# Performance work log

Hardware: AMD Instinct MI355X
Metric: run time of the kernel (lower is better)

The kernel has to match this reference:

```python
import jax, jax.numpy as jnp
import numpy as np

B, T, D_IN = 8, 1024, 320
L, H, DK, DV, DM, DI = 6, 8, 64, 64, 512, 2048


def _pe_table():
    pos = np.arange(T, dtype=np.float32)[:, None]
    div = np.exp(np.arange(0, DM, 2, dtype=np.float32) * (-np.log(10000.0) / DM))
    pe = np.zeros((T, DM), np.float32)
    pe[:, 0::2] = np.sin(pos * div)
    pe[:, 1::2] = np.cos(pos * div)
    return jnp.asarray(pe)


def setup_inputs() -> dict:
    key = jax.random.key(0)
    ks = jax.random.split(key, 16)
    rn = lambda k, shape, std: (jax.random.normal(k, shape, jnp.float32) * std)
    inp = {}
    inp["padded_input"] = jax.random.normal(ks[0], (B, T, D_IN), jnp.float32)
    inp["input_lengths"] = jax.random.randint(ks[1], (B,), T // 2, T + 1)
    # input projection + input layernorm (weights stored as [in, out])
    inp["w_in"] = rn(ks[2], (D_IN, DM), 0.02)
    inp["b_in"] = jnp.zeros((DM,), jnp.float32)
    inp["ln_in_g"] = jnp.ones((DM,), jnp.float32)
    inp["ln_in_b"] = jnp.zeros((DM,), jnp.float32)
    inp["pe"] = _pe_table()
    # stacked per-layer params, leading dim L
    inp["wq"] = rn(ks[3], (L, DM, H * DK), np.sqrt(2.0 / (DM + DK)))
    inp["bq"] = jnp.zeros((L, H * DK), jnp.float32)
    inp["wk"] = rn(ks[4], (L, DM, H * DK), np.sqrt(2.0 / (DM + DK)))
    inp["bk"] = jnp.zeros((L, H * DK), jnp.float32)
    inp["wv"] = rn(ks[5], (L, DM, H * DV), np.sqrt(2.0 / (DM + DV)))
    inp["bv"] = jnp.zeros((L, H * DV), jnp.float32)
    inp["wfc"] = rn(ks[6], (L, H * DV, DM), np.sqrt(2.0 / (H * DV + DM)))
    inp["bfc"] = jnp.zeros((L, DM), jnp.float32)
    inp["ln1_g"] = jnp.ones((L, DM), jnp.float32)
    inp["ln1_b"] = jnp.zeros((L, DM), jnp.float32)
    inp["w1"] = rn(ks[7], (L, DM, DI), np.sqrt(2.0 / (DM + DI)))
    inp["b1"] = jnp.zeros((L, DI), jnp.float32)
    inp["w2"] = rn(ks[8], (L, DI, DM), np.sqrt(2.0 / (DM + DI)))
    inp["b2"] = jnp.zeros((L, DM), jnp.float32)
    inp["ln2_g"] = jnp.ones((L, DM), jnp.float32)
    inp["ln2_b"] = jnp.zeros((L, DM), jnp.float32)
    return inp


def _layer_norm(x, g, b):
    mu = jnp.mean(x, axis=-1, keepdims=True)
    var = jnp.var(x, axis=-1, keepdims=True)
    return (x - mu) * jax.lax.rsqrt(var + 1e-5) * g + b


def _encoder(padded_input, input_lengths, w_in, b_in, ln_in_g, ln_in_b, pe,
             wq, bq, wk, bk, wv, bv, wfc, bfc, ln1_g, ln1_b,
             w1, b1, w2, b2, ln2_g, ln2_b):
    pos = jnp.arange(T)
    key_pad = pos[None, :] >= input_lengths[:, None]          # [B,T] True at pad
    non_pad = (~key_pad).astype(padded_input.dtype)[:, :, None]  # [B,T,1]
    scale = 1.0 / jnp.sqrt(jnp.float32(DK))

    x = _layer_norm(padded_input @ w_in + b_in, ln_in_g, ln_in_b) + pe[None]

    def body(x, p):
        Wq, Bq, Wk, Bk, Wv, Bv, Wfc, Bfc, G1, Bn1, W1, Bf1, W2, Bf2, G2, Bn2 = p
        res = x
        q = (x @ Wq + Bq).reshape(B, T, H, DK)
        k = (x @ Wk + Bk).reshape(B, T, H, DK)
        v = (x @ Wv + Bv).reshape(B, T, H, DV)
        attn = jnp.einsum('bqhd,bkhd->bhqk', q, k) * scale
        attn = jnp.where(key_pad[:, None, None, :], -jnp.inf, attn)
        attn = jax.nn.softmax(attn, axis=-1)
        o = jnp.einsum('bhqk,bkhd->bqhd', attn, v).reshape(B, T, H * DV)
        x = _layer_norm(o @ Wfc + Bfc + res, G1, Bn1) * non_pad
        res = x
        h = jax.nn.relu(x @ W1 + Bf1)
        x = _layer_norm(h @ W2 + Bf2 + res, G2, Bn2) * non_pad
        return x, None

    x, _ = jax.lax.scan(body, x, (wq, bq, wk, bk, wv, bv, wfc, bfc,
                                  ln1_g, ln1_b, w1, b1, w2, b2, ln2_g, ln2_b))
    return x


def reference(padded_input, input_lengths, w_in, b_in, ln_in_g, ln_in_b, pe,
              wq, bq, wk, bk, wv, bv, wfc, bfc, ln1_g, ln1_b,
              w1, b1, w2, b2, ln2_g, ln2_b):
    # dropout is identity in eval mode
    return _encoder(padded_input, input_lengths, w_in, b_in, ln_in_g, ln_in_b, pe,
                    wq, bq, wk, bk, wv, bv, wfc, bfc, ln1_g, ln1_b,
                    w1, b1, w2, b2, ln2_g, ln2_b)
```

## Files before the change

kernel.cpp:

```cpp
#include <hip/hip_runtime.h>
#include <hip/hip_bf16.h>


typedef unsigned short bh16;
typedef __bf16 bf16x8 __attribute__((ext_vector_type(8)));
typedef float f32x4 __attribute__((ext_vector_type(4)));
typedef unsigned int u32x4 __attribute__((ext_vector_type(4)));
typedef unsigned int u32x2 __attribute__((ext_vector_type(2)));

#define DEVI static __device__ __forceinline__

DEVI bh16 f2bf(float f) {
  union { float f; unsigned u; } x; x.f = f;
  unsigned r = x.u + 0x7fffu + ((x.u >> 16) & 1u);
  return (bh16)(r >> 16);
}
DEVI float bf2f(bh16 u) {
  union { unsigned u; float f; } x; x.u = ((unsigned)u) << 16; return x.f;
}
DEVI bf16x8 ld16(const bh16* p) {
  return __builtin_bit_cast(bf16x8, *(const u32x4*)p);
}
DEVI bf16x8 ld16b(const char* p) {
  return __builtin_bit_cast(bf16x8, *(const u32x4*)p);
}
DEVI f32x4 mfma16(bf16x8 a, bf16x8 b, f32x4 c) {
  return __builtin_amdgcn_mfma_f32_16x16x32_bf16(a, b, c, 0, 0, 0);
}
DEVI void async16(const void* g, void* l) {
  __builtin_amdgcn_global_load_lds(
      (const __attribute__((address_space(1))) void*)g,
      (__attribute__((address_space(3))) void*)l, 16, 0, 0);
}

DEVI void tcvt_body(const float* in, bh16* out, int K, int N, int n0, int k0) {
  __shared__ float t[32][33];
  int tx = threadIdx.x & 31, ty = threadIdx.x >> 5;
#pragma unroll
  for (int i = 0; i < 4; i++)
    t[ty + 8 * i][tx] = in[(size_t)(k0 + ty + 8 * i) * N + n0 + tx];
  __syncthreads();
#pragma unroll
  for (int i = 0; i < 4; i++)
    out[(size_t)(n0 + ty + 8 * i) * K + k0 + tx] = f2bf(t[tx][ty + 8 * i]);
}

__global__ __launch_bounds__(256) void tcvt_all(
    const float* __restrict__ w_in, const float* __restrict__ wq,
    const float* __restrict__ wk, const float* __restrict__ wv,
    const float* __restrict__ wfc, const float* __restrict__ w1,
    const float* __restrict__ w2, bh16* __restrict__ WinT,
    bh16* __restrict__ WqkvT, bh16* __restrict__ WfcT,
    bh16* __restrict__ W1T, bh16* __restrict__ W2T) {
  int p = blockIdx.x;
  const float* in; bh16* out; int K, N, rem;
  if (p < 160) {
    in = w_in; out = WinT; K = 320; N = 512; rem = p;
  } else if (p < 160 + 1536) {
    rem = p - 160; int l = rem >> 8; rem &= 255;
    in = wq + (size_t)l * 512 * 512; out = WqkvT + (size_t)l * 1536 * 512;
    K = 512; N = 512;
  } else if (p < 160 + 3072) {
    rem = p - 160 - 1536; int l = rem >> 8; rem &= 255;
    in = wk + (size_t)l * 512 * 512;
    out = WqkvT + (size_t)l * 1536 * 512 + (size_t)512 * 512;
    K = 512; N = 512;
  } else if (p < 160 + 4608) {
    rem = p - 160 - 3072; int l = rem >> 8; rem &= 255;
    in = wv + (size_t)l * 512 * 512;
    out = WqkvT + (size_t)l * 1536 * 512 + (size_t)1024 * 512;
    K = 512; N = 512;
  } else if (p < 160 + 6144) {
    rem = p - 160 - 4608; int l = rem >> 8; rem &= 255;
    in = wfc + (size_t)l * 512 * 512; out = WfcT + (size_t)l * 512 * 512;
    K = 512; N = 512;
  } else if (p < 160 + 6144 + 6144) {
    rem = p - 160 - 6144; int l = rem >> 10; rem &= 1023;
    in = w1 + (size_t)l * 512 * 2048; out = W1T + (size_t)l * 2048 * 512;
    K = 512; N = 2048;
  } else {
    rem = p - 160 - 12288; int l = rem >> 10; rem &= 1023;
    in = w2 + (size_t)l * 2048 * 512; out = W2T + (size_t)l * 512 * 2048;
    K = 2048; N = 512;
  }
  int nt = N >> 5;
  int n0 = (rem % nt) * 32, k0 = (rem / nt) * 32;
  tcvt_body(in, out, K, N, n0, k0);
}

__global__ __launch_bounds__(256) void bcat(
    const float* __restrict__ bq, const float* __restrict__ bk,
    const float* __restrict__ bv, float* __restrict__ out) {
  int l = blockIdx.x;
  for (int j = threadIdx.x; j < 1536; j += 256) {
    float v = (j < 512) ? bq[l * 512 + j]
            : (j < 1024) ? bk[l * 512 + j - 512] : bv[l * 512 + j - 1024];
    out[l * 1536 + j] = v;
  }
}

__global__ __launch_bounds__(256) void cvt_in(
    const float* __restrict__ in, bh16* __restrict__ out, int n4) {
  int i = blockIdx.x * 256 + threadIdx.x;
  if (i < n4) {
    float4 v = ((const float4*)in)[i];
    u32x2 pk;
    pk[0] = (unsigned)f2bf(v.x) | ((unsigned)f2bf(v.y) << 16);
    pk[1] = (unsigned)f2bf(v.z) | ((unsigned)f2bf(v.w) << 16);
    *(u32x2*)(out + (size_t)i * 4) = pk;
  }
}

template <int BM, int BN, int RELU, int OUTF32, int QKV>
__global__ __launch_bounds__(256) void gemm_bt(
    const bh16* __restrict__ A, const bh16* __restrict__ Bt,
    const float* __restrict__ bias, void* __restrict__ Cout,
    bh16* __restrict__ vtOut, const int* __restrict__ lens,
    int M, int N, int K) {
  constexpr int BK = 64;
  constexpr int PX = (8192 / BM) / 8;
  constexpr int PXS = (PX == 8) ? 3 : 4;
  __shared__ __align__(16) bh16 As[2][BM * BK];
  __shared__ __align__(16) bh16 Bs[2][BN * BK];
  const int tid = threadIdx.x;
  const int wave = tid >> 6, lane = tid & 63;
  const int lq = lane & 15, grp = lane >> 4;
  const int p = blockIdx.x;
  const int xcd = p & 7, idx = p >> 3;
  const int m0 = (((idx & (PX - 1)) << 3) | xcd) * BM;
  const int n0 = (idx >> PXS) * BN;
  if ((m0 & 1023) >= lens[m0 >> 10]) return;
  constexpr int FM = BM / 32, FN = BN / 32;
  const int wr = wave >> 1, wc = wave & 1;
  f32x4 acc[FM][FN] = {};

  const int nk = K / BK;
  auto stage = [&](int buf, int kt) {
#pragma unroll
    for (int i = 0; i < BM / 32; ++i) {
      int off = i * 4096 + wave * 1024 + lane * 16;
      int row = off >> 7, col = off & 127;
      int sw = (row & 7) << 4;
      const char* g =
          (const char*)A + ((size_t)(m0 + row) * K + kt * BK) * 2 + (col ^ sw);
      async16(g, (char*)As[buf] + off);
    }
#pragma unroll
    for (int i = 0; i < BN / 32; ++i) {
      int off = i * 4096 + wave * 1024 + lane * 16;
      int row = off >> 7, col = off & 127;
      int sw = (row & 7) << 4;
      const char* g =
          (const char*)Bt + ((size_t)(n0 + row) * K + kt * BK) * 2 + (col ^ sw);
      async16(g, (char*)Bs[buf] + off);
    }
  };

  stage(0, 0);
  for (int kt = 0; kt < nk; ++kt) {
    int cur = kt & 1;
    __syncthreads();
    if (kt + 1 < nk) stage(cur ^ 1, kt + 1);
#pragma unroll
    for (int kk = 0; kk < 2; ++kk) {
      bf16x8 af[FM], bfr[FN];
#pragma unroll
      for (int i = 0; i < FM; ++i) {
        int row = wr * (BM / 2) + i * 16 + lq;
        int sw = (row & 7) << 4;
        af[i] = ld16b((char*)As[cur] + row * 128 + ((kk * 64 + grp * 16) ^ sw));
      }
#pragma unroll
      for (int j = 0; j < FN; ++j) {
        int row = wc * (BN / 2) + j * 16 + lq;
        int sw = (row & 7) << 4;
        bfr[j] = ld16b((char*)Bs[cur] + row * 128 + ((kk * 64 + grp * 16) ^ sw));
      }
      __builtin_amdgcn_s_setprio(1);
#pragma unroll
      for (int i = 0; i < FM; ++i)
#pragma unroll
        for (int j = 0; j < FN; ++j)
          acc[i][j] = mfma16(af[i], bfr[j], acc[i][j]);
      __builtin_amdgcn_s_setprio(0);
    }
  }
  if (QKV && n0 >= 1024) {
#pragma unroll
    for (int i = 0; i < FM; ++i) {
#pragma unroll
      for (int j = 0; j < FN; ++j) {
        int col = n0 + wc * (BN / 2) + j * 16 + lq;
        float bv = bias[col];
        int vc = col - 1024;
        int t0 = m0 + wr * (BM / 2) + i * 16 + grp * 4;
        int bb = t0 >> 10, tl = t0 & 1023;
        u32x2 pk;
        pk[0] = (unsigned)f2bf(acc[i][j][0] + bv) |
                ((unsigned)f2bf(acc[i][j][1] + bv) << 16);
        pk[1] = (unsigned)f2bf(acc[i][j][2] + bv) |
                ((unsigned)f2bf(acc[i][j][3] + bv) << 16);
        *(u32x2*)&vtOut[((size_t)(bb * 512 + vc)) * 1024 + tl] = pk;
      }
    }
    return;
  }
#pragma unroll
  for (int i = 0; i < FM; ++i) {
#pragma unroll
    for (int j = 0; j < FN; ++j) {
      int col = n0 + wc * (BN / 2) + j * 16 + lq;
      float bv = bias[col];
#pragma unroll
      for (int r = 0; r < 4; ++r) {
        int row = m0 + wr * (BM / 2) + i * 16 + grp * 4 + r;
        float v = acc[i][j][r] + bv;
        if (RELU) v = fmaxf(v, 0.f);
        if (OUTF32) ((float*)Cout)[(size_t)row * N + col] = v;
        else ((bh16*)Cout)[(size_t)row * N + col] = f2bf(v);
      }
    }
  }
}

__global__ __launch_bounds__(256) void ln_pe_k(
    const float* __restrict__ in, const float* __restrict__ g,
    const float* __restrict__ bta, const float* __restrict__ pe,
    bh16* __restrict__ xb) {
  int wave = threadIdx.x >> 6, lane = threadIdx.x & 63;
  int row = blockIdx.x * 4 + wave;
  int t = row & 1023;
  const float* xr = in + (size_t)row * 512 + lane * 8;
  float4 a0 = ((const float4*)xr)[0], a1 = ((const float4*)xr)[1];
  float v[8] = {a0.x, a0.y, a0.z, a0.w, a1.x, a1.y, a1.z, a1.w};
  float s = 0.f, ss = 0.f;
#pragma unroll
  for (int j = 0; j < 8; j++) { s += v[j]; ss += v[j] * v[j]; }
#pragma unroll
  for (int m = 1; m < 64; m <<= 1) { s += __shfl_xor(s, m); ss += __shfl_xor(ss, m); }
  float mu = s * (1.f / 512.f);
  float rstd = rsqrtf(ss * (1.f / 512.f) - mu * mu + 1e-5f);
  int c0 = lane * 8;
  float o[8];
  u32x4 pk;
#pragma unroll
  for (int j = 0; j < 8; j++) {
    int c = c0 + j;
    o[j] = (v[j] - mu) * rstd * g[c] + bta[c] + pe[(size_t)t * 512 + c];
  }
#pragma unroll
  for (int j = 0; j < 4; j++)
    pk[j] = (unsigned)f2bf(o[2 * j]) | ((unsigned)f2bf(o[2 * j + 1]) << 16);
  *(u32x4*)(xb + (size_t)row * 512 + c0) = pk;
}

__global__ __launch_bounds__(256) void ln_res_k(
    const bh16* __restrict__ gout, const bh16* res,
    const float* __restrict__ g, const float* __restrict__ bta,
    const int* __restrict__ lens, bh16* xb, float* fout) {
  int wave = threadIdx.x >> 6, lane = threadIdx.x & 63;
  int row = blockIdx.x * 4 + wave;
  int b = row >> 10, t = row & 1023;
  float nonpad = (t < lens[b]) ? 1.f : 0.f;
  int c0 = lane * 8;
  u32x4 graw = *(const u32x4*)(gout + (size_t)row * 512 + c0);
  u32x4 rraw = *(const u32x4*)(res + (size_t)row * 512 + c0);
  float v[8];
#pragma unroll
  for (int j = 0; j < 4; j++) {
    v[2 * j] = bf2f((bh16)(graw[j] & 0xffffu)) + bf2f((bh16)(rraw[j] & 0xffffu));
    v[2 * j + 1] = bf2f((bh16)(graw[j] >> 16)) + bf2f((bh16)(rraw[j] >> 16));
  }
  float s = 0.f, ss = 0.f;
#pragma unroll
  for (int j = 0; j < 8; j++) { s += v[j]; ss += v[j] * v[j]; }
#pragma unroll
  for (int m = 1; m < 64; m <<= 1) { s += __shfl_xor(s, m); ss += __shfl_xor(ss, m); }
  float mu = s * (1.f / 512.f);
  float rstd = rsqrtf(ss * (1.f / 512.f) - mu * mu + 1e-5f);
  float o[8];
  u32x4 pk;
#pragma unroll
  for (int j = 0; j < 8; j++) {
    int c = c0 + j;
    o[j] = ((v[j] - mu) * rstd * g[c] + bta[c]) * nonpad;
  }
#pragma unroll
  for (int j = 0; j < 4; j++)
    pk[j] = (unsigned)f2bf(o[2 * j]) | ((unsigned)f2bf(o[2 * j + 1]) << 16);
  *(u32x4*)(xb + (size_t)row * 512 + c0) = pk;
  if (fout) {
    float4* xo = (float4*)(fout + (size_t)row * 512 + c0);
    xo[0] = make_float4(o[0], o[1], o[2], o[3]);
    xo[1] = make_float4(o[4], o[5], o[6], o[7]);
  }
}

__global__ __launch_bounds__(512) void attn_k(
    const bh16* __restrict__ qkv, const bh16* __restrict__ vt,
    const int* __restrict__ lens, bh16* __restrict__ o) {
  constexpr int LDP = 72;
  __shared__ __align__(16) char Ks[2][8192];
  __shared__ __align__(16) char Vs[2][8192];
  __shared__ __align__(16) bh16 P[8][16 * LDP];
  int p = blockIdx.x;
  int xcd = p & 7, s = p >> 3;
  int bh = ((s & 7) << 3) | xcd;
  int qt = s >> 3;
  int b = bh >> 3, h = bh & 7;
  int len = lens[b];
  if (qt * 128 >= len) return;
  int tid = threadIdx.x;
  int wave = tid >> 6, lane = tid & 63;
  int lq = lane & 15, grp = lane >> 4;

  size_t qrow = (size_t)(b * 1024 + qt * 128 + wave * 16 + lq);
  const bh16* Qp = qkv + qrow * 1536 + h * 64;
  bf16x8 qf0 = ld16(Qp + grp * 8);
  bf16x8 qf1 = ld16(Qp + 32 + grp * 8);
  const char* Kbase = (const char*)(qkv + (size_t)(b * 1024) * 1536 + 512 + h * 64);
  const char* Vbase = (const char*)(vt + (size_t)(bh * 64) * 1024);
  bh16* Pw = P[wave];

  f32x4 oacc[4] = {};
  float m = -1e30f, lsum = 0.f;
  int nkb = (len + 63) >> 6;

  auto stage = [&](int buf, int kb) {
    int off = tid * 16;
    int row = off >> 7, cb = off & 127;
    int sw = (row & 7) << 4;
    async16(Kbase + (size_t)(kb * 64 + row) * 3072 + (cb ^ sw), Ks[buf] + off);
    async16(Vbase + (size_t)row * 2048 + kb * 128 + (cb ^ sw), Vs[buf] + off);
  };

  stage(0, 0);
  for (int kb = 0; kb < nkb; ++kb) {
    int cur = kb & 1;
    __syncthreads();
    if (kb + 1 < nkb) stage(cur ^ 1, kb + 1);
    int k64 = kb * 64;
    f32x4 st[4];
    __builtin_amdgcn_s_setprio(1);
#pragma unroll
    for (int sv = 0; sv < 4; ++sv) {
      int row = sv * 16 + lq, sw = (row & 7) << 4;
      const char* kp = Ks[cur] + row * 128;
      f32x4 z = {};
      z = mfma16(ld16b(kp + ((grp * 16) ^ sw)), qf0, z);
      z = mfma16(ld16b(kp + ((64 + grp * 16) ^ sw)), qf1, z);
      st[sv] = z;
    }
    __builtin_amdgcn_s_setprio(0);
    float tmax = -1e30f;
    if (k64 + 64 > len) {
#pragma unroll
      for (int sv = 0; sv < 4; ++sv)
#pragma unroll
        for (int r = 0; r < 4; ++r) {
          int key = k64 + sv * 16 + grp * 4 + r;
          float v = st[sv][r] * 0.125f;
          v = (key < len) ? v : -1e30f;
          st[sv][r] = v;
          tmax = fmaxf(tmax, v);
        }
    } else {
#pragma unroll
      for (int sv = 0; sv < 4; ++sv)
#pragma unroll
        for (int r = 0; r < 4; ++r) {
          float v = st[sv][r] * 0.125f;
          st[sv][r] = v;
          tmax = fmaxf(tmax, v);
        }
    }
    tmax = fmaxf(tmax, __shfl_xor(tmax, 16));
    tmax = fmaxf(tmax, __shfl_xor(tmax, 32));
    float newm = fmaxf(m, tmax);
    if (!__all(newm - m <= 8.f)) {
      float sc = __expf(m - newm);
      m = newm;
      lsum *= sc;
#pragma unroll
      for (int r = 0; r < 4; ++r) {
        float scr = __shfl(sc, grp * 4 + r);
#pragma unroll
        for (int dt = 0; dt < 4; ++dt) oacc[dt][r] *= scr;
      }
    }
    float rs = 0.f;
#pragma unroll
    for (int sv = 0; sv < 4; ++sv) {
      float p0 = __expf(st[sv][0] - m), p1 = __expf(st[sv][1] - m);
      float p2 = __expf(st[sv][2] - m), p3 = __expf(st[sv][3] - m);
      rs += (p0 + p1) + (p2 + p3);
      u32x2 pk;
      pk[0] = (unsigned)f2bf(p0) | ((unsigned)f2bf(p1) << 16);
      pk[1] = (unsigned)f2bf(p2) | ((unsigned)f2bf(p3) << 16);
      *(u32x2*)&Pw[lq * LDP + sv * 16 + grp * 4] = pk;
    }
    rs += __shfl_xor(rs, 16);
    rs += __shfl_xor(rs, 32);
    lsum += rs;
#pragma unroll
    for (int kk = 0; kk < 2; ++kk) {
      bf16x8 pa = ld16(Pw + lq * LDP + kk * 32 + grp * 8);
      __builtin_amdgcn_s_setprio(1);
#pragma unroll
      for (int dt = 0; dt < 4; ++dt) {
        int row = dt * 16 + lq, sw = (row & 7) << 4;
        bf16x8 vfr = ld16b(Vs[cur] + row * 128 + ((kk * 64 + grp * 16) ^ sw));
        oacc[dt] = mfma16(pa, vfr, oacc[dt]);
      }
      __builtin_amdgcn_s_setprio(0);
    }
  }
#pragma unroll
  for (int r = 0; r < 4; ++r) {
    float li = __shfl(lsum, grp * 4 + r);
    float inv = 1.f / li;
    int row = qt * 128 + wave * 16 + grp * 4 + r;
    bh16* orow = o + (size_t)(b * 1024 + row) * 512 + h * 64;
#pragma unroll
    for (int dt = 0; dt < 4; ++dt) orow[dt * 16 + lq] = f2bf(oacc[dt][r] * inv);
  }
}

extern "C" void kernel_launch(void* const* d_in, const int* in_sizes, int n_in,
                              void* d_out, int out_size, void* d_ws, size_t ws_size,
                              hipStream_t stream) {
  const float* padded = (const float*)d_in[0];
  const int* lens = (const int*)d_in[1];
  const float* w_in = (const float*)d_in[2];
  const float* b_in = (const float*)d_in[3];
  const float* ln_in_g = (const float*)d_in[4];
  const float* ln_in_b = (const float*)d_in[5];
  const float* pe = (const float*)d_in[6];
  const float* wq = (const float*)d_in[7];
  const float* bq = (const float*)d_in[8];
  const float* wk = (const float*)d_in[9];
  const float* bk = (const float*)d_in[10];
  const float* wv = (const float*)d_in[11];
  const float* bv = (const float*)d_in[12];
  const float* wfc = (const float*)d_in[13];
  const float* bfc = (const float*)d_in[14];
  const float* ln1_g = (const float*)d_in[15];
  const float* ln1_b = (const float*)d_in[16];
  const float* w1 = (const float*)d_in[17];
  const float* b1 = (const float*)d_in[18];
  const float* w2 = (const float*)d_in[19];
  const float* b2 = (const float*)d_in[20];
  const float* ln2_g = (const float*)d_in[21];
  const float* ln2_b = (const float*)d_in[22];

  char* ws = (char*)d_ws;
  size_t off = 0;
  auto alloc = [&](size_t bytes) -> char* {
    char* p = ws + off;
    off += (bytes + 255) & ~(size_t)255;
    return p;
  };
  bh16* WinT  = (bh16*)alloc((size_t)512 * 320 * 2);
  bh16* WqkvT = (bh16*)alloc((size_t)6 * 1536 * 512 * 2);
  bh16* WfcT  = (bh16*)alloc((size_t)6 * 512 * 512 * 2);
  bh16* W1T   = (bh16*)alloc((size_t)6 * 2048 * 512 * 2);
  bh16* W2T   = (bh16*)alloc((size_t)6 * 512 * 2048 * 2);
  float* bqkv = (float*)alloc((size_t)6 * 1536 * 4);
  bh16* xb    = (bh16*)alloc((size_t)8192 * 512 * 2);
  bh16* qkvb  = (bh16*)alloc((size_t)8192 * 1536 * 2);
  bh16* vt    = (bh16*)alloc((size_t)64 * 64 * 1024 * 2);
  bh16* ob    = (bh16*)alloc((size_t)8192 * 512 * 2);
  float* tmp32 = (float*)alloc((size_t)8192 * 512 * 4);
  bh16* tmp16 = (bh16*)alloc((size_t)8192 * 512 * 2);
  bh16* hbuf  = (bh16*)alloc((size_t)8192 * 2048 * 2);
  bh16* padb  = hbuf;
  if (off > ws_size) return;

  tcvt_all<<<18592, 256, 0, stream>>>(w_in, wq, wk, wv, wfc, w1, w2,
                                      WinT, WqkvT, WfcT, W1T, W2T);
  bcat<<<6, 256, 0, stream>>>(bq, bk, bv, bqkv);
  cvt_in<<<2560, 256, 0, stream>>>(padded, padb, 655360);

  gemm_bt<128, 64, 0, 1, 0><<<512, 256, 0, stream>>>(
      padb, WinT, b_in, tmp32, nullptr, lens, 8192, 512, 320);
  ln_pe_k<<<2048, 256, 0, stream>>>(tmp32, ln_in_g, ln_in_b, pe, xb);

  for (int l = 0; l < 6; ++l) {
    gemm_bt<128, 128, 0, 0, 1><<<768, 256, 0, stream>>>(
        xb, WqkvT + (size_t)l * 1536 * 512, bqkv + l * 1536, qkvb, vt, lens,
        8192, 1536, 512);
    attn_k<<<512, 512, 0, stream>>>(qkvb, vt, lens, ob);
    gemm_bt<64, 64, 0, 0, 0><<<1024, 256, 0, stream>>>(
        ob, WfcT + (size_t)l * 512 * 512, bfc + l * 512, tmp16, nullptr, lens,
        8192, 512, 512);
    ln_res_k<<<2048, 256, 0, stream>>>(tmp16, xb, ln1_g + l * 512, ln1_b + l * 512,
                                       lens, xb, nullptr);
    gemm_bt<64, 128, 1, 0, 0><<<2048, 256, 0, stream>>>(
        xb, W1T + (size_t)l * 2048 * 512, b1 + l * 2048, hbuf, nullptr, lens,
        8192, 2048, 512);
    gemm_bt<64, 64, 0, 0, 0><<<1024, 256, 0, stream>>>(
        hbuf, W2T + (size_t)l * 512 * 2048, b2 + l * 512, tmp16, nullptr, lens,
        8192, 512, 2048);
    ln_res_k<<<2048, 256, 0, stream>>>(tmp16, xb, ln2_g + l * 512, ln2_b + l * 512,
                                       lens, xb, (l == 5) ? (float*)d_out : nullptr);
  }
}
```

Measured before the change: 803.1 us.

## Split-K the FFN down-projection and fuse partial sums into residual layernorm

```diff
diff --git a/kernel.cpp b/kernel.cpp
--- a/kernel.cpp
+++ b/kernel.cpp
@@ -111,7 +111,7 @@
   }
 }
 
-template <int BM, int BN, int RELU, int OUTF32, int QKV>
+template <int BM, int BN, int RELU, int OUTF32, int QKV, int SPLITK = 1>
 __global__ __launch_bounds__(256) void gemm_bt(
     const bh16* __restrict__ A, const bh16* __restrict__ Bt,
     const float* __restrict__ bias, void* __restrict__ Cout,
@@ -125,7 +125,12 @@
   const int tid = threadIdx.x;
   const int wave = tid >> 6, lane = tid & 63;
   const int lq = lane & 15, grp = lane >> 4;
-  const int p = blockIdx.x;
+  int p = blockIdx.x;
+  int s2 = 0;
+  if (SPLITK == 2) {
+    int half = gridDim.x >> 1;
+    if (p >= half) { s2 = 1; p -= half; }
+  }
   const int xcd = p & 7, idx = p >> 3;
   const int m0 = (((idx & (PX - 1)) << 3) | xcd) * BM;
   const int n0 = (idx >> PXS) * BN;
@@ -134,15 +139,16 @@
   const int wr = wave >> 1, wc = wave & 1;
   f32x4 acc[FM][FN] = {};
 
-  const int nk = K / BK;
-  auto stage = [&](int buf, int kt) {
+  const int nk = K / BK / SPLITK;
+  const int kb0 = s2 * nk;
+  auto stage = [&](int buf, int ktg) {
 #pragma unroll
     for (int i = 0; i < BM / 32; ++i) {
       int off = i * 4096 + wave * 1024 + lane * 16;
       int row = off >> 7, col = off & 127;
       int sw = (row & 7) << 4;
       const char* g =
-          (const char*)A + ((size_t)(m0 + row) * K + kt * BK) * 2 + (col ^ sw);
+          (const char*)A + ((size_t)(m0 + row) * K + ktg * BK) * 2 + (col ^ sw);
       async16(g, (char*)As[buf] + off);
     }
 #pragma unroll
@@ -151,16 +157,16 @@
       int row = off >> 7, col = off & 127;
       int sw = (row & 7) << 4;
       const char* g =
-          (const char*)Bt + ((size_t)(n0 + row) * K + kt * BK) * 2 + (col ^ sw);
+          (const char*)Bt + ((size_t)(n0 + row) * K + ktg * BK) * 2 + (col ^ sw);
       async16(g, (char*)Bs[buf] + off);
     }
   };
 
-  stage(0, 0);
+  stage(0, kb0);
   for (int kt = 0; kt < nk; ++kt) {
     int cur = kt & 1;
     __syncthreads();
-    if (kt + 1 < nk) stage(cur ^ 1, kt + 1);
+    if (kt + 1 < nk) stage(cur ^ 1, kb0 + kt + 1);
 #pragma unroll
     for (int kk = 0; kk < 2; ++kk) {
       bf16x8 af[FM], bfr[FN];
@@ -205,18 +211,19 @@
     }
     return;
   }
+  float* fbase = (float*)Cout + (SPLITK == 2 ? (size_t)s2 * M * N : 0);
 #pragma unroll
   for (int i = 0; i < FM; ++i) {
 #pragma unroll
     for (int j = 0; j < FN; ++j) {
       int col = n0 + wc * (BN / 2) + j * 16 + lq;
-      float bv = bias[col];
+      float bv = (SPLITK == 2 && s2) ? 0.f : bias[col];
 #pragma unroll
       for (int r = 0; r < 4; ++r) {
         int row = m0 + wr * (BM / 2) + i * 16 + grp * 4 + r;
         float v = acc[i][j][r] + bv;
         if (RELU) v = fmaxf(v, 0.f);
-        if (OUTF32) ((float*)Cout)[(size_t)row * N + col] = v;
+        if (OUTF32) fbase[(size_t)row * N + col] = v;
         else ((bh16*)Cout)[(size_t)row * N + col] = f2bf(v);
       }
     }
@@ -224,15 +231,20 @@
 }
 
 __global__ __launch_bounds__(256) void ln_pe_k(
-    const float* __restrict__ in, const float* __restrict__ g,
+    const bh16* __restrict__ in, const float* __restrict__ g,
     const float* __restrict__ bta, const float* __restrict__ pe,
     bh16* __restrict__ xb) {
   int wave = threadIdx.x >> 6, lane = threadIdx.x & 63;
   int row = blockIdx.x * 4 + wave;
   int t = row & 1023;
-  const float* xr = in + (size_t)row * 512 + lane * 8;
-  float4 a0 = ((const float4*)xr)[0], a1 = ((const float4*)xr)[1];
-  float v[8] = {a0.x, a0.y, a0.z, a0.w, a1.x, a1.y, a1.z, a1.w};
+  int c0 = lane * 8;
+  u32x4 raw = *(const u32x4*)(in + (size_t)row * 512 + c0);
+  float v[8];
+#pragma unroll
+  for (int j = 0; j < 4; j++) {
+    v[2 * j] = bf2f((bh16)(raw[j] & 0xffffu));
+    v[2 * j + 1] = bf2f((bh16)(raw[j] >> 16));
+  }
   float s = 0.f, ss = 0.f;
 #pragma unroll
   for (int j = 0; j < 8; j++) { s += v[j]; ss += v[j] * v[j]; }
@@ -240,7 +252,6 @@
   for (int m = 1; m < 64; m <<= 1) { s += __shfl_xor(s, m); ss += __shfl_xor(ss, m); }
   float mu = s * (1.f / 512.f);
   float rstd = rsqrtf(ss * (1.f / 512.f) - mu * mu + 1e-5f);
-  int c0 = lane * 8;
   float o[8];
   u32x4 pk;
 #pragma unroll
@@ -270,6 +281,53 @@
   for (int j = 0; j < 4; j++) {
     v[2 * j] = bf2f((bh16)(graw[j] & 0xffffu)) + bf2f((bh16)(rraw[j] & 0xffffu));
     v[2 * j + 1] = bf2f((bh16)(graw[j] >> 16)) + bf2f((bh16)(rraw[j] >> 16));
+  }
+  float s = 0.f, ss = 0.f;
+#pragma unroll
+  for (int j = 0; j < 8; j++) { s += v[j]; ss += v[j] * v[j]; }
+#pragma unroll
+  for (int m = 1; m < 64; m <<= 1) { s += __shfl_xor(s, m); ss += __shfl_xor(ss, m); }
+  float mu = s * (1.f / 512.f);
+  float rstd = rsqrtf(ss * (1.f / 512.f) - mu * mu + 1e-5f);
+  float o[8];
+  u32x4 pk;
+#pragma unroll
+  for (int j = 0; j < 8; j++) {
+    int c = c0 + j;
+    o[j] = ((v[j] - mu) * rstd * g[c] + bta[c]) * nonpad;
+  }
+#pragma unroll
+  for (int j = 0; j < 4; j++)
+    pk[j] = (unsigned)f2bf(o[2 * j]) | ((unsigned)f2bf(o[2 * j + 1]) << 16);
+  *(u32x4*)(xb + (size_t)row * 512 + c0) = pk;
+  if (fout) {
+    float4* xo = (float4*)(fout + (size_t)row * 512 + c0);
+    xo[0] = make_float4(o[0], o[1], o[2], o[3]);
+    xo[1] = make_float4(o[4], o[5], o[6], o[7]);
+  }
+}
+
+__global__ __launch_bounds__(256) void ln2_res_k(
+    const float* __restrict__ g0, const float* __restrict__ g1,
+    const bh16* res, const float* __restrict__ g,
+    const float* __restrict__ bta, const int* __restrict__ lens,
+    bh16* xb, float* fout) {
+  int wave = threadIdx.x >> 6, lane = threadIdx.x & 63;
+  int row = blockIdx.x * 4 + wave;
+  int b = row >> 10, t = row & 1023;
+  float nonpad = (t < lens[b]) ? 1.f : 0.f;
+  int c0 = lane * 8;
+  const float* p0 = g0 + (size_t)row * 512 + c0;
+  const float* p1 = g1 + (size_t)row * 512 + c0;
+  float4 a0 = ((const float4*)p0)[0], a1 = ((const float4*)p0)[1];
+  float4 b0 = ((const float4*)p1)[0], b1 = ((const float4*)p1)[1];
+  u32x4 rraw = *(const u32x4*)(res + (size_t)row * 512 + c0);
+  float v[8] = {a0.x + b0.x, a0.y + b0.y, a0.z + b0.z, a0.w + b0.w,
+                a1.x + b1.x, a1.y + b1.y, a1.z + b1.z, a1.w + b1.w};
+#pragma unroll
+  for (int j = 0; j < 4; j++) {
+    v[2 * j] += bf2f((bh16)(rraw[j] & 0xffffu));
+    v[2 * j + 1] += bf2f((bh16)(rraw[j] >> 16));
   }
   float s = 0.f, ss = 0.f;
 #pragma unroll
@@ -470,7 +528,7 @@
   bh16* qkvb  = (bh16*)alloc((size_t)8192 * 1536 * 2);
   bh16* vt    = (bh16*)alloc((size_t)64 * 64 * 1024 * 2);
   bh16* ob    = (bh16*)alloc((size_t)8192 * 512 * 2);
-  float* tmp32 = (float*)alloc((size_t)8192 * 512 * 4);
+  float* tmp32 = (float*)alloc((size_t)2 * 8192 * 512 * 4);
   bh16* tmp16 = (bh16*)alloc((size_t)8192 * 512 * 2);
   bh16* hbuf  = (bh16*)alloc((size_t)8192 * 2048 * 2);
   bh16* padb  = hbuf;
@@ -481,12 +539,12 @@
   bcat<<<6, 256, 0, stream>>>(bq, bk, bv, bqkv);
   cvt_in<<<2560, 256, 0, stream>>>(padded, padb, 655360);
 
-  gemm_bt<128, 64, 0, 1, 0><<<512, 256, 0, stream>>>(
-      padb, WinT, b_in, tmp32, nullptr, lens, 8192, 512, 320);
-  ln_pe_k<<<2048, 256, 0, stream>>>(tmp32, ln_in_g, ln_in_b, pe, xb);
+  gemm_bt<64, 64, 0, 0, 0><<<1024, 256, 0, stream>>>(
+      padb, WinT, b_in, tmp16, nullptr, lens, 8192, 512, 320);
+  ln_pe_k<<<2048, 256, 0, stream>>>(tmp16, ln_in_g, ln_in_b, pe, xb);
 
   for (int l = 0; l < 6; ++l) {
-    gemm_bt<128, 128, 0, 0, 1><<<768, 256, 0, stream>>>(
+    gemm_bt<64, 128, 0, 0, 1><<<1536, 256, 0, stream>>>(
         xb, WqkvT + (size_t)l * 1536 * 512, bqkv + l * 1536, qkvb, vt, lens,
         8192, 1536, 512);
     attn_k<<<512, 512, 0, stream>>>(qkvb, vt, lens, ob);
@@ -498,10 +556,11 @@
     gemm_bt<64, 128, 1, 0, 0><<<2048, 256, 0, stream>>>(
         xb, W1T + (size_t)l * 2048 * 512, b1 + l * 2048, hbuf, nullptr, lens,
         8192, 2048, 512);
-    gemm_bt<64, 64, 0, 0, 0><<<1024, 256, 0, stream>>>(
-        hbuf, W2T + (size_t)l * 512 * 2048, b2 + l * 512, tmp16, nullptr, lens,
+    gemm_bt<64, 64, 0, 1, 0, 2><<<2048, 256, 0, stream>>>(
+        hbuf, W2T + (size_t)l * 512 * 2048, b2 + l * 512, tmp32, nullptr, lens,
         8192, 512, 2048);
-    ln_res_k<<<2048, 256, 0, stream>>>(tmp16, xb, ln2_g + l * 512, ln2_b + l * 512,
-                                       lens, xb, (l == 5) ? (float*)d_out : nullptr);
-  }
-}
+    ln2_res_k<<<2048, 256, 0, stream>>>(tmp32, tmp32 + (size_t)8192 * 512, xb,
+                                        ln2_g + l * 512, ln2_b + l * 512,
+                                        lens, xb, (l == 5) ? (float*)d_out : nullptr);
+  }
+}
```

Measured after the change: 819.3 us. 1.02x slower.
